# Kernel optimization log

Measured on AMD Instinct MI355X. Metric: run time of the kernel, lower is better.

## Reference

```python
import jax, jax.numpy as jnp
import numpy as np

HEADS = 8
DIM_HEAD = 64
SCALE = DIM_HEAD ** -0.5


def setup_inputs() -> dict:
    key = jax.random.key(0)
    k1, k2, k3 = jax.random.split(key, 3)
    b, p, n, dim = 2, 16, 512, 512
    inner = HEADS * DIM_HEAD  # 512
    x = jax.random.normal(k1, (b, p, n, dim), dtype=jnp.float32)
    W_qkv = jax.random.normal(k2, (dim, 3 * inner), dtype=jnp.float32) * (dim ** -0.5)
    W_out = jax.random.normal(k3, (inner, dim), dtype=jnp.float32) * (inner ** -0.5)
    b_out = jnp.zeros((dim,), dtype=jnp.float32)
    return {"x": x, "W_qkv": W_qkv, "W_out": W_out, "b_out": b_out}


def reference(x, W_qkv, W_out, b_out):
    b, p, n, dim = x.shape
    # QKV projection (no bias), split into q, k, v
    qkv = jnp.einsum('bpnd,de->bpne', x, W_qkv)
    q, k, v = jnp.split(qkv, 3, axis=-1)
    # (b, p, n, h*d) -> (b, p, h, n, d)
    def to_heads(t):
        return t.reshape(b, p, n, HEADS, DIM_HEAD).transpose(0, 1, 3, 2, 4)
    q, k, v = to_heads(q), to_heads(k), to_heads(v)
    # attention scores: (b, p, h, n, n)
    dots = jnp.einsum('bphnd,bphmd->bphnm', q, k) * SCALE
    attn = jax.nn.softmax(dots, axis=-1)
    out = jnp.einsum('bphnm,bphmd->bphnd', attn, v)
    # (b, p, h, n, d) -> (b, p, n, h*d)
    out = out.transpose(0, 1, 3, 2, 4).reshape(b, p, n, HEADS * DIM_HEAD)
    # output projection (dropout rate = 0.0 -> identity)
    return jnp.einsum('bpne,ed->bpnd', out, W_out) + b_out
```

## Files before the change

### kernel.cpp

```cpp
#include <hip/hip_runtime.h>
#include <hip/hip_bf16.h>

typedef short bf16x8 __attribute__((ext_vector_type(8)));
typedef short bf16x4 __attribute__((ext_vector_type(4)));
typedef float f32x4  __attribute__((ext_vector_type(4)));

__device__ __forceinline__ unsigned short f2bf(float f) {
    union { float fv; unsigned int u; } v; v.fv = f;
    unsigned int r = v.u + 0x7FFFu + ((v.u >> 16) & 1u);
    return (unsigned short)(r >> 16);
}

__device__ __forceinline__ void gload16(const short* g, short* l) {
    __builtin_amdgcn_global_load_lds(
        (const __attribute__((address_space(1))) void*)g,
        (__attribute__((address_space(3))) void*)l, 16, 0, 0);
}

__global__ __launch_bounds__(256) void cvt_x(
    const float* __restrict__ x, short* __restrict__ xb)
{
    size_t i = ((size_t)blockIdx.x * 256 + threadIdx.x) * 8;
    f32x4 a = *(const f32x4*)(x + i);
    f32x4 b = *(const f32x4*)(x + i + 4);
    bf16x8 s;
    #pragma unroll
    for (int e = 0; e < 4; ++e) { s[e] = (short)f2bf(a[e]); s[4 + e] = (short)f2bf(b[e]); }
    *(bf16x8*)(xb + i) = s;
}

__global__ __launch_bounds__(256) void prep_w(
    const float* __restrict__ Wqkv, const float* __restrict__ Wout,
    short* __restrict__ Wqkvt, short* __restrict__ Woutt)
{
    int idx = blockIdx.x * 256 + threadIdx.x;
    int n = idx >> 9, k = idx & 511;
    Wqkvt[idx] = (short)f2bf(Wqkv[(size_t)k * 1536 + n]);
    if (idx < 512 * 512) {
        Woutt[idx] = (short)f2bf(Wout[(size_t)k * 512 + n]);
    }
}

template<int F32OUT>
__global__ __launch_bounds__(256, 2) void gemm_db(
    const short* __restrict__ A, const short* __restrict__ Bt,
    short* __restrict__ Cb, float* __restrict__ Cf, const float* __restrict__ bias,
    int M, int N, int K, int NB)
{
    __shared__ short lds[2][2][128 * 64];
    const int t    = threadIdx.x;
    const int lane = t & 63;
    const int wid  = t >> 6;
    const int l15  = lane & 15;
    const int lg   = lane >> 4;

    const int cpx = gridDim.x >> 3;
    const int swz = (blockIdx.x & 7) * cpx + (blockIdx.x >> 3);
    const int m0 = (swz / NB) * 128;
    const int n0 = (swz % NB) * 128;

    const int wm = (wid >> 1) * 64;
    const int wn = (wid & 1) * 64;

    const int scol = 8 * ((lane & 7) ^ ((lane >> 3) & 7));

    float bval[4];
    if constexpr (F32OUT) {
        #pragma unroll
        for (int ni = 0; ni < 4; ++ni) bval[ni] = bias[n0 + wn + ni * 16 + l15];
    }

    f32x4 acc[4][4];
    #pragma unroll
    for (int i = 0; i < 4; ++i)
        #pragma unroll
        for (int j = 0; j < 4; ++j)
            acc[i][j] = f32x4{0.f, 0.f, 0.f, 0.f};

    const int NT = K >> 6;

    auto stage = [&](int buf, int tk) {
        #pragma unroll
        for (int j = 0; j < 4; ++j) {
            const int r = wid * 32 + j * 8 + (lane >> 3);
            gload16(A  + (size_t)(m0 + r) * K + tk * 64 + scol,
                    &lds[buf][0][(wid * 32 + j * 8) * 64]);
            gload16(Bt + (size_t)(n0 + r) * K + tk * 64 + scol,
                    &lds[buf][1][(wid * 32 + j * 8) * 64]);
        }
    };

    stage(0, 0);

    for (int tk = 0; tk < NT; ++tk) {
        const int cur = tk & 1;
        if (tk + 1 < NT) {
            stage(cur ^ 1, tk + 1);
            asm volatile("s_waitcnt vmcnt(8)" ::: "memory");
        } else {
            asm volatile("s_waitcnt vmcnt(0)" ::: "memory");
        }
        __builtin_amdgcn_s_barrier();

        bf16x8 af[4][2], bg[4][2];
        #pragma unroll
        for (int kk = 0; kk < 2; ++kk) {
            #pragma unroll
            for (int mi = 0; mi < 4; ++mi)
                af[mi][kk] = *(const bf16x8*)&lds[cur][0][
                    (wm + mi * 16 + l15) * 64 + (((kk * 4 + lg) ^ (l15 & 7)) * 8)];
            #pragma unroll
            for (int ni = 0; ni < 4; ++ni)
                bg[ni][kk] = *(const bf16x8*)&lds[cur][1][
                    (wn + ni * 16 + l15) * 64 + (((kk * 4 + lg) ^ (l15 & 7)) * 8)];
        }

        __builtin_amdgcn_s_setprio(1);
        #pragma unroll
        for (int kk = 0; kk < 2; ++kk)
            #pragma unroll
            for (int mi = 0; mi < 4; ++mi)
                #pragma unroll
                for (int ni = 0; ni < 4; ++ni)
                    acc[mi][ni] = __builtin_amdgcn_mfma_f32_16x16x32_bf16(
                        af[mi][kk], bg[ni][kk], acc[mi][ni], 0, 0, 0);
        __builtin_amdgcn_s_setprio(0);
        __builtin_amdgcn_s_barrier();
    }

    #pragma unroll
    for (int mi = 0; mi < 4; ++mi) {
        #pragma unroll
        for (int ni = 0; ni < 4; ++ni) {
            const int col = n0 + wn + ni * 16 + l15;
            #pragma unroll
            for (int r = 0; r < 4; ++r) {
                const int rowi = m0 + wm + mi * 16 + 4 * lg + r;
                if constexpr (F32OUT) {
                    Cf[(size_t)rowi * N + col] = acc[mi][ni][r] + bval[ni];
                } else {
                    Cb[(size_t)rowi * N + col] = (short)f2bf(acc[mi][ni][r]);
                }
            }
        }
    }
}

__global__ __launch_bounds__(512) void attn_kernel(
    const short* __restrict__ qkv, short* __restrict__ attn_out)
{
    __shared__ short Kl[64][72];
    __shared__ short Vt[64][76];
    const int t    = threadIdx.x;
    const int lane = t & 63;
    const int wid  = t >> 6;
    const int l15  = lane & 15;
    const int lg   = lane >> 4;
    const int bph = blockIdx.x;
    const int bp = bph >> 3, h = bph & 7;
    const size_t tok0 = (size_t)bp * 512;
    const int q0   = wid * 64;
    const int qcol = h * 64;

    bf16x8 qf[4][2];
    #pragma unroll
    for (int mj = 0; mj < 4; ++mj)
        #pragma unroll
        for (int kf = 0; kf < 2; ++kf)
            qf[mj][kf] = *(const bf16x8*)(qkv + (tok0 + q0 + mj * 16 + l15) * 1536
                                          + qcol + kf * 32 + 8 * lg);

    f32x4 ot[4][4];
    #pragma unroll
    for (int i = 0; i < 4; ++i)
        #pragma unroll
        for (int j = 0; j < 4; ++j)
            ot[i][j] = f32x4{0.f, 0.f, 0.f, 0.f};
    float mrun[4], lrun[4];
    #pragma unroll
    for (int mj = 0; mj < 4; ++mj) { mrun[mj] = -1e30f; lrun[mj] = 0.f; }

    const int sn = t >> 3;
    const int sd = (t & 7) * 8;

    for (int kv0 = 0; kv0 < 512; kv0 += 64) {
        const short* kvrow = qkv + (tok0 + kv0 + sn) * 1536;
        *(bf16x8*)&Kl[sn][sd] = *(const bf16x8*)(kvrow + 512 + qcol + sd);
        bf16x8 vv = *(const bf16x8*)(kvrow + 1024 + qcol + sd);
        #pragma unroll
        for (int i = 0; i < 8; ++i) Vt[sd + i][sn] = vv[i];
        __syncthreads();

        f32x4 st[4][4];
        #pragma unroll
        for (int i = 0; i < 4; ++i)
            #pragma unroll
            for (int j = 0; j < 4; ++j)
                st[i][j] = f32x4{0.f, 0.f, 0.f, 0.f};
        #pragma unroll
        for (int kf = 0; kf < 2; ++kf) {
            #pragma unroll
            for (int ni = 0; ni < 4; ++ni) {
                bf16x8 kfr = *(const bf16x8*)&Kl[ni * 16 + l15][kf * 32 + 8 * lg];
                #pragma unroll
                for (int mj = 0; mj < 4; ++mj)
                    st[ni][mj] = __builtin_amdgcn_mfma_f32_16x16x32_bf16(
                        kfr, qf[mj][kf], st[ni][mj], 0, 0, 0);
            }
        }

        #pragma unroll
        for (int mj = 0; mj < 4; ++mj) {
            float pm = -1e30f;
            #pragma unroll
            for (int ni = 0; ni < 4; ++ni)
                #pragma unroll
                for (int r = 0; r < 4; ++r) {
                    st[ni][mj][r] *= 0.125f;
                    pm = fmaxf(pm, st[ni][mj][r]);
                }
            pm = fmaxf(pm, __shfl_xor(pm, 16));
            pm = fmaxf(pm, __shfl_xor(pm, 32));
            const float mnew = fmaxf(mrun[mj], pm);
            const float fsc  = __expf(mrun[mj] - mnew);
            float ps = 0.f;
            #pragma unroll
            for (int ni = 0; ni < 4; ++ni)
                #pragma unroll
                for (int r = 0; r < 4; ++r) {
                    float e = __expf(st[ni][mj][r] - mnew);
                    st[ni][mj][r] = e;
                    ps += e;
                }
            ps += __shfl_xor(ps, 16);
            ps += __shfl_xor(ps, 32);
            lrun[mj] = lrun[mj] * fsc + ps;
            mrun[mj] = mnew;
            #pragma unroll
            for (int di = 0; di < 4; ++di)
                ot[di][mj] *= fsc;
        }

        #pragma unroll
        for (int ni = 0; ni < 4; ++ni) {
            bf16x4 pb[4];
            #pragma unroll
            for (int mj = 0; mj < 4; ++mj)
                #pragma unroll
                for (int r = 0; r < 4; ++r)
                    pb[mj][r] = (short)f2bf(st[ni][mj][r]);
            #pragma unroll
            for (int di = 0; di < 4; ++di) {
                bf16x4 av = *(const bf16x4*)&Vt[di * 16 + l15][ni * 16 + 4 * lg];
                #pragma unroll
                for (int mj = 0; mj < 4; ++mj)
                    ot[di][mj] = __builtin_amdgcn_mfma_f32_16x16x16bf16_1k(
                        av, pb[mj], ot[di][mj], 0, 0, 0);
            }
        }
        __syncthreads();
    }

    float inv[4];
    #pragma unroll
    for (int mj = 0; mj < 4; ++mj) inv[mj] = 1.f / lrun[mj];
    #pragma unroll
    for (int di = 0; di < 4; ++di)
        #pragma unroll
        for (int mj = 0; mj < 4; ++mj) {
            const size_t tok = tok0 + q0 + mj * 16 + l15;
            const int col = qcol + di * 16 + 4 * lg;
            bf16x4 o4;
            #pragma unroll
            for (int r = 0; r < 4; ++r)
                o4[r] = (short)f2bf(ot[di][mj][r] * inv[mj]);
            *(bf16x4*)(attn_out + tok * 512 + col) = o4;
        }
}

extern "C" void kernel_launch(void* const* d_in, const int* in_sizes, int n_in,
                              void* d_out, int out_size, void* d_ws, size_t ws_size,
                              hipStream_t stream) {
    const float* x    = (const float*)d_in[0];
    const float* Wqkv = (const float*)d_in[1];
    const float* Wout = (const float*)d_in[2];
    const float* bout = (const float*)d_in[3];
    float* out = (float*)d_out;

    char* ws = (char*)d_ws;
    short* qkvb  = (short*)(ws);
    short* xb    = (short*)(ws + 50331648ull);
    short* attnb = xb;
    short* Wqkvt = (short*)(ws + 67108864ull);
    short* Woutt = (short*)(ws + 68681728ull);

    cvt_x<<<4096, 256, 0, stream>>>(x, xb);
    prep_w<<<3072, 256, 0, stream>>>(Wqkv, Wout, Wqkvt, Woutt);

    gemm_db<0><<<1536, 256, 0, stream>>>(xb, Wqkvt, qkvb, nullptr, nullptr,
                                         16384, 1536, 512, 12);

    attn_kernel<<<256, 512, 0, stream>>>(qkvb, attnb);

    gemm_db<1><<<512, 256, 0, stream>>>(attnb, Woutt, nullptr, out, bout,
                                        16384, 512, 512, 4);
}
```

Baseline: 106.2 us.

## Split attention queries across two blocks, double-buffer K/V, add lazy softmax rescaling

The attention kernel now launches 512 blocks, each handling 256 queries with 32 per wave, instead of 256 blocks of 512 queries. This doubles the parallelism across CUs and halves the per-wave registers. K/V tiles are double-buffered in LDS, with the next tile prefetched into registers, which removes one barrier per iteration. Softmax switches to exp2 with a log2e-folded scale and only rescales the accumulators when the row max grows by more than a threshold. In exchange, K/V is loaded twice per (b,p,h) pair and LDS use doubles.

```diff
diff --git a/kernel.cpp b/kernel.cpp
--- a/kernel.cpp
+++ b/kernel.cpp
@@ -146,128 +146,140 @@
     }
 }
 
-__global__ __launch_bounds__(512) void attn_kernel(
+__global__ __launch_bounds__(512, 4) void attn_kernel(
     const short* __restrict__ qkv, short* __restrict__ attn_out)
 {
-    __shared__ short Kl[64][72];
-    __shared__ short Vt[64][76];
+    __shared__ short Kl[2][64][72];
+    __shared__ short Vt[2][64][76];
     const int t    = threadIdx.x;
     const int lane = t & 63;
     const int wid  = t >> 6;
     const int l15  = lane & 15;
     const int lg   = lane >> 4;
-    const int bph = blockIdx.x;
-    const int bp = bph >> 3, h = bph & 7;
+    const int pairid = blockIdx.x & 255;
+    const int qh  = blockIdx.x >> 8;
+    const int bp  = pairid >> 3;
+    const int h   = pairid & 7;
     const size_t tok0 = (size_t)bp * 512;
-    const int q0   = wid * 64;
+    const int q0   = qh * 256 + wid * 32;
     const int qcol = h * 64;
 
-    bf16x8 qf[4][2];
-    #pragma unroll
-    for (int mj = 0; mj < 4; ++mj)
+    bf16x8 qf[2][2];
+    #pragma unroll
+    for (int mj = 0; mj < 2; ++mj)
         #pragma unroll
         for (int kf = 0; kf < 2; ++kf)
             qf[mj][kf] = *(const bf16x8*)(qkv + (tok0 + q0 + mj * 16 + l15) * 1536
                                           + qcol + kf * 32 + 8 * lg);
 
-    f32x4 ot[4][4];
+    f32x4 ot[4][2];
     #pragma unroll
     for (int i = 0; i < 4; ++i)
         #pragma unroll
-        for (int j = 0; j < 4; ++j)
+        for (int j = 0; j < 2; ++j)
             ot[i][j] = f32x4{0.f, 0.f, 0.f, 0.f};
-    float mrun[4], lrun[4];
-    #pragma unroll
-    for (int mj = 0; mj < 4; ++mj) { mrun[mj] = -1e30f; lrun[mj] = 0.f; }
+    float mrun[2] = {-1e30f, -1e30f}, lrun[2] = {0.f, 0.f};
 
     const int sn = t >> 3;
     const int sd = (t & 7) * 8;
 
-    for (int kv0 = 0; kv0 < 512; kv0 += 64) {
-        const short* kvrow = qkv + (tok0 + kv0 + sn) * 1536;
-        *(bf16x8*)&Kl[sn][sd] = *(const bf16x8*)(kvrow + 512 + qcol + sd);
-        bf16x8 vv = *(const bf16x8*)(kvrow + 1024 + qcol + sd);
-        #pragma unroll
-        for (int i = 0; i < 8; ++i) Vt[sd + i][sn] = vv[i];
+    const short* kvbase = qkv + (tok0 + sn) * 1536 + qcol + sd;
+    bf16x8 kreg = *(const bf16x8*)(kvbase + 512);
+    bf16x8 vreg = *(const bf16x8*)(kvbase + 1024);
+
+    const float C = 0.18033688011112042f;
+
+    for (int tkv = 0; tkv < 8; ++tkv) {
+        const int cur = tkv & 1;
+        *(bf16x8*)&Kl[cur][sn][sd] = kreg;
+        #pragma unroll
+        for (int i = 0; i < 8; ++i) Vt[cur][sd + i][sn] = vreg[i];
+        if (tkv < 7) {
+            const short* nxt = kvbase + (size_t)(tkv + 1) * 64 * 1536;
+            kreg = *(const bf16x8*)(nxt + 512);
+            vreg = *(const bf16x8*)(nxt + 1024);
+        }
         __syncthreads();
 
-        f32x4 st[4][4];
+        f32x4 st[4][2];
         #pragma unroll
         for (int i = 0; i < 4; ++i)
             #pragma unroll
-            for (int j = 0; j < 4; ++j)
+            for (int j = 0; j < 2; ++j)
                 st[i][j] = f32x4{0.f, 0.f, 0.f, 0.f};
         #pragma unroll
         for (int kf = 0; kf < 2; ++kf) {
             #pragma unroll
             for (int ni = 0; ni < 4; ++ni) {
-                bf16x8 kfr = *(const bf16x8*)&Kl[ni * 16 + l15][kf * 32 + 8 * lg];
-                #pragma unroll
-                for (int mj = 0; mj < 4; ++mj)
+                bf16x8 kfr = *(const bf16x8*)&Kl[cur][ni * 16 + l15][kf * 32 + 8 * lg];
+                #pragma unroll
+                for (int mj = 0; mj < 2; ++mj)
                     st[ni][mj] = __builtin_amdgcn_mfma_f32_16x16x32_bf16(
                         kfr, qf[mj][kf], st[ni][mj], 0, 0, 0);
             }
         }
 
         #pragma unroll
-        for (int mj = 0; mj < 4; ++mj) {
+        for (int mj = 0; mj < 2; ++mj) {
             float pm = -1e30f;
             #pragma unroll
             for (int ni = 0; ni < 4; ++ni)
                 #pragma unroll
                 for (int r = 0; r < 4; ++r) {
-                    st[ni][mj][r] *= 0.125f;
+                    st[ni][mj][r] *= C;
                     pm = fmaxf(pm, st[ni][mj][r]);
                 }
             pm = fmaxf(pm, __shfl_xor(pm, 16));
             pm = fmaxf(pm, __shfl_xor(pm, 32));
-            const float mnew = fmaxf(mrun[mj], pm);
-            const float fsc  = __expf(mrun[mj] - mnew);
+            if (!__all(pm <= mrun[mj] + 8.f)) {
+                const float mnew = fmaxf(mrun[mj], pm);
+                const float fsc  = __builtin_amdgcn_exp2f(mrun[mj] - mnew);
+                lrun[mj] *= fsc;
+                #pragma unroll
+                for (int di = 0; di < 4; ++di)
+                    ot[di][mj] *= fsc;
+                mrun[mj] = mnew;
+            }
             float ps = 0.f;
             #pragma unroll
             for (int ni = 0; ni < 4; ++ni)
                 #pragma unroll
                 for (int r = 0; r < 4; ++r) {
-                    float e = __expf(st[ni][mj][r] - mnew);
+                    float e = __builtin_amdgcn_exp2f(st[ni][mj][r] - mrun[mj]);
                     st[ni][mj][r] = e;
                     ps += e;
                 }
             ps += __shfl_xor(ps, 16);
             ps += __shfl_xor(ps, 32);
-            lrun[mj] = lrun[mj] * fsc + ps;
-            mrun[mj] = mnew;
-            #pragma unroll
-            for (int di = 0; di < 4; ++di)
-                ot[di][mj] *= fsc;
+            lrun[mj] += ps;
         }
 
         #pragma unroll
         for (int ni = 0; ni < 4; ++ni) {
-            bf16x4 pb[4];
-            #pragma unroll
-            for (int mj = 0; mj < 4; ++mj)
+            bf16x4 pb[2];
+            #pragma unroll
+            for (int mj = 0; mj < 2; ++mj)
                 #pragma unroll
                 for (int r = 0; r < 4; ++r)
                     pb[mj][r] = (short)f2bf(st[ni][mj][r]);
             #pragma unroll
             for (int di = 0; di < 4; ++di) {
-                bf16x4 av = *(const bf16x4*)&Vt[di * 16 + l15][ni * 16 + 4 * lg];
-                #pragma unroll
-                for (int mj = 0; mj < 4; ++mj)
+                bf16x4 av = *(const bf16x4*)&Vt[cur][di * 16 + l15][ni * 16 + 4 * lg];
+                #pragma unroll
+                for (int mj = 0; mj < 2; ++mj)
                     ot[di][mj] = __builtin_amdgcn_mfma_f32_16x16x16bf16_1k(
                         av, pb[mj], ot[di][mj], 0, 0, 0);
             }
         }
-        __syncthreads();
-    }
-
-    float inv[4];
-    #pragma unroll
-    for (int mj = 0; mj < 4; ++mj) inv[mj] = 1.f / lrun[mj];
+    }
+
+    float inv[2];
+    #pragma unroll
+    for (int mj = 0; mj < 2; ++mj) inv[mj] = 1.f / lrun[mj];
     #pragma unroll
     for (int di = 0; di < 4; ++di)
         #pragma unroll
-        for (int mj = 0; mj < 4; ++mj) {
+        for (int mj = 0; mj < 2; ++mj) {
             const size_t tok = tok0 + q0 + mj * 16 + l15;
             const int col = qcol + di * 16 + 4 * lg;
             bf16x4 o4;
@@ -300,7 +312,7 @@
     gemm_db<0><<<1536, 256, 0, stream>>>(xb, Wqkvt, qkvb, nullptr, nullptr,
                                          16384, 1536, 512, 12);
 
-    attn_kernel<<<256, 512, 0, stream>>>(qkvb, attnb);
+    attn_kernel<<<512, 512, 0, stream>>>(qkvb, attnb);
 
     gemm_db<1><<<512, 256, 0, stream>>>(attnb, Woutt, nullptr, out, bout,
                                         16384, 512, 512, 4);
```

Measured after the change: 103.3 us. 2.8% less time.
